# Kernel tuning notes

Measured on AMD Instinct MI355X. Metric: run time of the kernel, lower is better.

Reference implementation:

```python
import jax, jax.numpy as jnp
import numpy as np


def setup_inputs() -> dict:
    key = jax.random.key(0)
    k1, k2 = jax.random.split(key)
    B, G, P = 32, 64, 256
    pred_patches = jax.random.normal(k1, (B, G, P, 3), dtype=jnp.float32)
    target_patches = jax.random.normal(k2, (B, G, P, 3), dtype=jnp.float32)
    return {"pred_patches": pred_patches, "target_patches": target_patches}


def reference(pred_patches, target_patches):
    b, g, p, _ = pred_patches.shape
    pred = pred_patches.reshape(b * g, p, 3)    # (BG, P, 3)
    tgt = target_patches.reshape(b * g, p, 3)   # (BG, P, 3)
    # Squared euclidean distance via ||p||^2 + ||q||^2 - 2 p.q (matches cdist(p=2)**2)
    pn = jnp.sum(pred * pred, axis=-1)          # (BG, P)
    tn = jnp.sum(tgt * tgt, axis=-1)            # (BG, P)
    cross = jnp.einsum('bpd,bqd->bpq', pred, tgt)  # (BG, P, P)
    dist2 = jnp.maximum(pn[:, :, None] + tn[:, None, :] - 2.0 * cross, 0.0)
    forward_dist = jnp.min(dist2, axis=2).mean(axis=1)   # nearest target for each pred point
    backward_dist = jnp.min(dist2, axis=1).mean(axis=1)  # nearest pred for each target point
    per_patch = forward_dist + backward_dist             # (BG,)
    return jnp.mean(per_patch)  # reduction='mean' over batch*patches
```

## Files before the change

kernel.cpp:

```cpp
#include <hip/hip_runtime.h>


#define NPATCH 2048
#define NPTS   256

typedef float v4f __attribute__((ext_vector_type(4)));

__global__ __launch_bounds__(256, 4) void chamfer_patch_kernel(
    const float* __restrict__ pred,
    const float* __restrict__ tgt,
    float* __restrict__ partial)
{
    __shared__ float sP[4][NPTS];
    __shared__ float sT[4][NPTS];
    __shared__ float mhalf[2][NPTS];
    __shared__ float red[2];

    const int patch = blockIdx.x;
    const int tid   = threadIdx.x;

    {
        const float* __restrict__ pb = pred + (size_t)patch * (NPTS * 3);
        const float* __restrict__ tb = tgt  + (size_t)patch * (NPTS * 3);
        float x = pb[3 * tid + 0], y = pb[3 * tid + 1], z = pb[3 * tid + 2];
        sP[0][tid] = x; sP[1][tid] = y; sP[2][tid] = z;
        sP[3][tid] = fmaf(z, z, fmaf(y, y, x * x));
        x = tb[3 * tid + 0]; y = tb[3 * tid + 1]; z = tb[3 * tid + 2];
        sT[0][tid] = x; sT[1][tid] = y; sT[2][tid] = z;
        sT[3][tid] = fmaf(z, z, fmaf(y, y, x * x));
    }
    __syncthreads();

    const int wave = tid >> 6;
    const int lane = tid & 63;
    const int dir  = wave >> 1;
    const int half = wave & 1;

    const float (*Q)[NPTS] = (dir == 0) ? sP : sT;
    const float (*S)[NPTS] = (dir == 0) ? sT : sP;

    float qx[4], qy[4], qz[4], qn[4], m[4];
#pragma unroll
    for (int q = 0; q < 4; ++q) {
        const int p = lane + 64 * q;
        qx[q] = -2.0f * Q[0][p];
        qy[q] = -2.0f * Q[1][p];
        qz[q] = -2.0f * Q[2][p];
        qn[q] = Q[3][p];
        m[q]  = 1e30f;
    }

    const int jbase = half * (NPTS / 2);
    const float* __restrict__ Sx = &S[0][jbase];
    const float* __restrict__ Sy = &S[1][jbase];
    const float* __restrict__ Sz = &S[2][jbase];
    const float* __restrict__ Sn = &S[3][jbase];

#pragma unroll 4
    for (int jj = 0; jj < NPTS / 2; jj += 4) {
        const v4f x4 = *(const v4f*)(Sx + jj);
        const v4f y4 = *(const v4f*)(Sy + jj);
        const v4f z4 = *(const v4f*)(Sz + jj);
        const v4f n4 = *(const v4f*)(Sn + jj);
#pragma unroll
        for (int q = 0; q < 4; ++q) {
            const float da = fmaf(qx[q], x4.x, fmaf(qy[q], y4.x, fmaf(qz[q], z4.x, n4.x)));
            const float db = fmaf(qx[q], x4.y, fmaf(qy[q], y4.y, fmaf(qz[q], z4.y, n4.y)));
            m[q] = fminf(m[q], fminf(da, db));
            const float dc = fmaf(qx[q], x4.z, fmaf(qy[q], y4.z, fmaf(qz[q], z4.z, n4.z)));
            const float dd = fmaf(qx[q], x4.w, fmaf(qy[q], y4.w, fmaf(qz[q], z4.w, n4.w)));
            m[q] = fminf(m[q], fminf(dc, dd));
        }
    }

    if (half == 1) {
#pragma unroll
        for (int q = 0; q < 4; ++q)
            mhalf[dir][lane + 64 * q] = m[q];
    }
    __syncthreads();

    if (half == 0) {
        float s = 0.0f;
#pragma unroll
        for (int q = 0; q < 4; ++q) {
            const float mm = fminf(m[q], mhalf[dir][lane + 64 * q]);
            s += fmaxf(qn[q] + mm, 0.0f);
        }
#pragma unroll
        for (int off = 32; off > 0; off >>= 1)
            s += __shfl_down(s, off, 64);
        if (lane == 0) red[dir] = s;
    }
    __syncthreads();
    if (tid == 0) partial[patch] = red[0] + red[1];
}

__global__ __launch_bounds__(256) void chamfer_reduce_kernel(
    const float* __restrict__ partial,
    float* __restrict__ out)
{
    __shared__ float red[4];
    const int tid = threadIdx.x;
    float s = 0.0f;
#pragma unroll
    for (int i = tid; i < NPATCH; i += 256) s += partial[i];
#pragma unroll
    for (int off = 32; off > 0; off >>= 1)
        s += __shfl_down(s, off, 64);
    if ((tid & 63) == 0) red[tid >> 6] = s;
    __syncthreads();
    if (tid == 0)
        out[0] = (red[0] + red[1] + red[2] + red[3]) *
                 (1.0f / ((float)NPTS * (float)NPATCH));
}

extern "C" void kernel_launch(void* const* d_in, const int* in_sizes, int n_in,
                              void* d_out, int out_size, void* d_ws, size_t ws_size,
                              hipStream_t stream) {
    const float* pred = (const float*)d_in[0];
    const float* tgt  = (const float*)d_in[1];
    float* partial    = (float*)d_ws;
    float* out        = (float*)d_out;

    chamfer_patch_kernel<<<NPATCH, 256, 0, stream>>>(pred, tgt, partial);
    chamfer_reduce_kernel<<<1, 256, 0, stream>>>(partial, out);
}
```

Baseline: 84.18 us.

## Fuse final reduction via atomicAdd and process two patches per block

Removes the separate single-block reduce kernel by having each block atomically add its scaled partial sum to the output, which is zeroed with a memset beforehand. Each block now loops over two patches, halving the grid to 1024 blocks. This saves a kernel launch and the serial tail of the reduce kernel. The cost is a less parallel grid, no overlap between a patch's global loads and the previous patch's compute, and a float summation order that depends on atomic timing.

```diff
diff --git a/kernel.cpp b/kernel.cpp
--- a/kernel.cpp
+++ b/kernel.cpp
@@ -6,113 +6,104 @@
 
 typedef float v4f __attribute__((ext_vector_type(4)));
 
-__global__ __launch_bounds__(256, 4) void chamfer_patch_kernel(
+__global__ __launch_bounds__(256, 4) void chamfer_kernel(
     const float* __restrict__ pred,
     const float* __restrict__ tgt,
-    float* __restrict__ partial)
+    float* __restrict__ out)
 {
     __shared__ float sP[4][NPTS];
     __shared__ float sT[4][NPTS];
     __shared__ float mhalf[2][NPTS];
     __shared__ float red[2];
 
-    const int patch = blockIdx.x;
-    const int tid   = threadIdx.x;
-
-    {
-        const float* __restrict__ pb = pred + (size_t)patch * (NPTS * 3);
-        const float* __restrict__ tb = tgt  + (size_t)patch * (NPTS * 3);
-        float x = pb[3 * tid + 0], y = pb[3 * tid + 1], z = pb[3 * tid + 2];
-        sP[0][tid] = x; sP[1][tid] = y; sP[2][tid] = z;
-        sP[3][tid] = fmaf(z, z, fmaf(y, y, x * x));
-        x = tb[3 * tid + 0]; y = tb[3 * tid + 1]; z = tb[3 * tid + 2];
-        sT[0][tid] = x; sT[1][tid] = y; sT[2][tid] = z;
-        sT[3][tid] = fmaf(z, z, fmaf(y, y, x * x));
-    }
-    __syncthreads();
-
+    const int tid  = threadIdx.x;
     const int wave = tid >> 6;
     const int lane = tid & 63;
     const int dir  = wave >> 1;
     const int half = wave & 1;
 
-    const float (*Q)[NPTS] = (dir == 0) ? sP : sT;
-    const float (*S)[NPTS] = (dir == 0) ? sT : sP;
+    float blocksum = 0.0f;
 
-    float qx[4], qy[4], qz[4], qn[4], m[4];
+#pragma unroll 1
+    for (int pp = 0; pp < 2; ++pp) {
+        const int patch = blockIdx.x * 2 + pp;
+
+        __syncthreads();
+
+        {
+            const float* __restrict__ pb = pred + (size_t)patch * (NPTS * 3);
+            const float* __restrict__ tb = tgt  + (size_t)patch * (NPTS * 3);
+            float x = pb[3 * tid + 0], y = pb[3 * tid + 1], z = pb[3 * tid + 2];
+            sP[0][tid] = x; sP[1][tid] = y; sP[2][tid] = z;
+            sP[3][tid] = fmaf(z, z, fmaf(y, y, x * x));
+            x = tb[3 * tid + 0]; y = tb[3 * tid + 1]; z = tb[3 * tid + 2];
+            sT[0][tid] = x; sT[1][tid] = y; sT[2][tid] = z;
+            sT[3][tid] = fmaf(z, z, fmaf(y, y, x * x));
+        }
+        __syncthreads();
+
+        const float (*Q)[NPTS] = (dir == 0) ? sP : sT;
+        const float (*S)[NPTS] = (dir == 0) ? sT : sP;
+
+        float qx[4], qy[4], qz[4], qn[4], m[4];
 #pragma unroll
-    for (int q = 0; q < 4; ++q) {
-        const int p = lane + 64 * q;
-        qx[q] = -2.0f * Q[0][p];
-        qy[q] = -2.0f * Q[1][p];
-        qz[q] = -2.0f * Q[2][p];
-        qn[q] = Q[3][p];
-        m[q]  = 1e30f;
+        for (int q = 0; q < 4; ++q) {
+            const int p = lane + 64 * q;
+            qx[q] = -2.0f * Q[0][p];
+            qy[q] = -2.0f * Q[1][p];
+            qz[q] = -2.0f * Q[2][p];
+            qn[q] = Q[3][p];
+            m[q]  = 1e30f;
+        }
+
+        const int jbase = half * (NPTS / 2);
+        const float* __restrict__ Sx = &S[0][jbase];
+        const float* __restrict__ Sy = &S[1][jbase];
+        const float* __restrict__ Sz = &S[2][jbase];
+        const float* __restrict__ Sn = &S[3][jbase];
+
+#pragma unroll 4
+        for (int jj = 0; jj < NPTS / 2; jj += 4) {
+            const v4f x4 = *(const v4f*)(Sx + jj);
+            const v4f y4 = *(const v4f*)(Sy + jj);
+            const v4f z4 = *(const v4f*)(Sz + jj);
+            const v4f n4 = *(const v4f*)(Sn + jj);
+#pragma unroll
+            for (int q = 0; q < 4; ++q) {
+                const float da = fmaf(qx[q], x4.x, fmaf(qy[q], y4.x, fmaf(qz[q], z4.x, n4.x)));
+                const float db = fmaf(qx[q], x4.y, fmaf(qy[q], y4.y, fmaf(qz[q], z4.y, n4.y)));
+                m[q] = fminf(m[q], fminf(da, db));
+                const float dc = fmaf(qx[q], x4.z, fmaf(qy[q], y4.z, fmaf(qz[q], z4.z, n4.z)));
+                const float dd = fmaf(qx[q], x4.w, fmaf(qy[q], y4.w, fmaf(qz[q], z4.w, n4.w)));
+                m[q] = fminf(m[q], fminf(dc, dd));
+            }
+        }
+
+        if (half == 1) {
+#pragma unroll
+            for (int q = 0; q < 4; ++q)
+                mhalf[dir][lane + 64 * q] = m[q];
+        }
+        __syncthreads();
+
+        if (half == 0) {
+            float s = 0.0f;
+#pragma unroll
+            for (int q = 0; q < 4; ++q) {
+                const float mm = fminf(m[q], mhalf[dir][lane + 64 * q]);
+                s += fmaxf(qn[q] + mm, 0.0f);
+            }
+#pragma unroll
+            for (int off = 32; off > 0; off >>= 1)
+                s += __shfl_down(s, off, 64);
+            if (lane == 0) red[dir] = s;
+        }
+        __syncthreads();
+        if (tid == 0) blocksum += red[0] + red[1];
     }
 
-    const int jbase = half * (NPTS / 2);
-    const float* __restrict__ Sx = &S[0][jbase];
-    const float* __restrict__ Sy = &S[1][jbase];
-    const float* __restrict__ Sz = &S[2][jbase];
-    const float* __restrict__ Sn = &S[3][jbase];
-
-#pragma unroll 4
-    for (int jj = 0; jj < NPTS / 2; jj += 4) {
-        const v4f x4 = *(const v4f*)(Sx + jj);
-        const v4f y4 = *(const v4f*)(Sy + jj);
-        const v4f z4 = *(const v4f*)(Sz + jj);
-        const v4f n4 = *(const v4f*)(Sn + jj);
-#pragma unroll
-        for (int q = 0; q < 4; ++q) {
-            const float da = fmaf(qx[q], x4.x, fmaf(qy[q], y4.x, fmaf(qz[q], z4.x, n4.x)));
-            const float db = fmaf(qx[q], x4.y, fmaf(qy[q], y4.y, fmaf(qz[q], z4.y, n4.y)));
-            m[q] = fminf(m[q], fminf(da, db));
-            const float dc = fmaf(qx[q], x4.z, fmaf(qy[q], y4.z, fmaf(qz[q], z4.z, n4.z)));
-            const float dd = fmaf(qx[q], x4.w, fmaf(qy[q], y4.w, fmaf(qz[q], z4.w, n4.w)));
-            m[q] = fminf(m[q], fminf(dc, dd));
-        }
-    }
-
-    if (half == 1) {
-#pragma unroll
-        for (int q = 0; q < 4; ++q)
-            mhalf[dir][lane + 64 * q] = m[q];
-    }
-    __syncthreads();
-
-    if (half == 0) {
-        float s = 0.0f;
-#pragma unroll
-        for (int q = 0; q < 4; ++q) {
-            const float mm = fminf(m[q], mhalf[dir][lane + 64 * q]);
-            s += fmaxf(qn[q] + mm, 0.0f);
-        }
-#pragma unroll
-        for (int off = 32; off > 0; off >>= 1)
-            s += __shfl_down(s, off, 64);
-        if (lane == 0) red[dir] = s;
-    }
-    __syncthreads();
-    if (tid == 0) partial[patch] = red[0] + red[1];
-}
-
-__global__ __launch_bounds__(256) void chamfer_reduce_kernel(
-    const float* __restrict__ partial,
-    float* __restrict__ out)
-{
-    __shared__ float red[4];
-    const int tid = threadIdx.x;
-    float s = 0.0f;
-#pragma unroll
-    for (int i = tid; i < NPATCH; i += 256) s += partial[i];
-#pragma unroll
-    for (int off = 32; off > 0; off >>= 1)
-        s += __shfl_down(s, off, 64);
-    if ((tid & 63) == 0) red[tid >> 6] = s;
-    __syncthreads();
     if (tid == 0)
-        out[0] = (red[0] + red[1] + red[2] + red[3]) *
-                 (1.0f / ((float)NPTS * (float)NPATCH));
+        atomicAdd(out, blocksum * (1.0f / ((float)NPTS * (float)NPATCH)));
 }
 
 extern "C" void kernel_launch(void* const* d_in, const int* in_sizes, int n_in,
@@ -120,9 +111,8 @@
                               hipStream_t stream) {
     const float* pred = (const float*)d_in[0];
     const float* tgt  = (const float*)d_in[1];
-    float* partial    = (float*)d_ws;
     float* out        = (float*)d_out;
 
-    chamfer_patch_kernel<<<NPATCH, 256, 0, stream>>>(pred, tgt, partial);
-    chamfer_reduce_kernel<<<1, 256, 0, stream>>>(partial, out);
+    hipMemsetAsync(out, 0, sizeof(float), stream);
+    chamfer_kernel<<<NPATCH / 2, 256, 0, stream>>>(pred, tgt, out);
 }
```

Result: slower. 87.23 us (+3.6%).
